# Kernel tuning notes

Hardware: AMD Instinct MI355X
Metric: run time of the kernel (lower is better)

The kernel has to match this reference:

```python
import jax, jax.numpy as jnp
import numpy as np
from jax import lax

B, S, H = 2, 2048, 768
FF = 1536
E = 8
TOP_K = 2


def setup_inputs() -> dict:
    key = jax.random.key(0)
    k1, k2, k3, k4 = jax.random.split(key, 4)
    hidden_states = jax.random.normal(k1, (B, S, H), dtype=jnp.float32)
    # torch init: weight.normal_() for experts; nn.Linear default init for gate (approx normal here is fine for a numerics baseline)
    gate_w = jax.random.normal(k2, (E, H), dtype=jnp.float32) * 0.02
    w_fc = jax.random.normal(k3, (E, FF, H), dtype=jnp.float32) * 0.02
    w_proj = jax.random.normal(k4, (E, H, FF), dtype=jnp.float32) * 0.02
    return {"hidden_states": hidden_states, "gate_w": gate_w, "w_fc": w_fc, "w_proj": w_proj}


def reference(hidden_states, gate_w, w_fc, w_proj):
    b, s, h = hidden_states.shape
    x = hidden_states.reshape(-1, h)                      # [T, H]
    # --- top-k gating (logits in float32, as in the torch code) ---
    logits = (x @ gate_w.T).astype(jnp.float32)           # [T, E]
    top_logits, top_idx = lax.top_k(logits, TOP_K)        # [T, K]
    gates = jax.nn.softmax(top_logits, axis=1).astype(x.dtype)  # [T, K]
    # combined per-token/per-expert gate: g[t,e] = sum_k gates[t,k]*[idx[t,k]==e]
    onehot = jax.nn.one_hot(top_idx, E, dtype=x.dtype)    # [T, K, E]
    g = jnp.einsum('tk,tke->te', gates, onehot)           # [T, E]
    # --- experts: gather + per-expert GEMM + gated scatter-add combine ---
    # Equivalent math: tokens with zero gate for expert e contribute nothing,
    # so compute each expert on all tokens and weight by g[:, e].
    out = jnp.zeros_like(x)
    for e in range(E):  # fixed small loop over experts (structurally distinct weights)
        hmid = jax.nn.gelu(x @ w_fc[e].T, approximate=False)   # [T, FF] (torch gelu = erf form)
        out = out + g[:, e:e + 1] * (hmid @ w_proj[e].T)       # [T, H]
    out = out.reshape(b, s, h)
    return out, logits
```

## Files before the change

kernel.cpp:

```cpp
#include <hip/hip_runtime.h>
#include <hip/hip_bf16.h>
#include <math.h>
#include <stdint.h>

#define TOKENS 4096
#define HDIM   768
#define FFDIM  1536
#define NEXP   8
#define MAXRT  72

typedef __attribute__((ext_vector_type(8))) short bf16x8;
typedef __attribute__((ext_vector_type(4))) float f32x4;

__device__ __forceinline__ unsigned short f2bf(float f) {
    union { float f; uint32_t u; } c; c.f = f;
    uint32_t u = c.u;
    uint32_t r = (u + 0x7FFFu + ((u >> 16) & 1u)) >> 16;
    return (unsigned short)r;
}

__device__ __forceinline__ void gload_lds16(const void* g, void* l) {
    __builtin_amdgcn_global_load_lds(
        (const __attribute__((address_space(1))) void*)g,
        (__attribute__((address_space(3))) void*)l, 16, 0, 0);
}

__global__ void cast_bf16_2(const float* __restrict__ s1, unsigned short* __restrict__ d1,
                            const float* __restrict__ s2, unsigned short* __restrict__ d2,
                            int n4) {
    int stride = gridDim.x * blockDim.x;
    for (int i = blockIdx.x * blockDim.x + threadIdx.x; i < 2 * n4; i += stride) {
        const float4* s = (i < n4) ? (const float4*)s1 : (const float4*)s2;
        ushort4* d = (i < n4) ? (ushort4*)d1 : (ushort4*)d2;
        int j = (i < n4) ? i : i - n4;
        float4 v = s[j];
        ushort4 o;
        o.x = f2bf(v.x); o.y = f2bf(v.y); o.z = f2bf(v.z); o.w = f2bf(v.w);
        d[j] = o;
    }
}

__global__ __launch_bounds__(256) void gating(
    const float* __restrict__ x, const float* __restrict__ gw,
    float* __restrict__ logits,
    int* __restrict__ tok_e, float* __restrict__ tok_g,
    unsigned short* __restrict__ x_bf, float* __restrict__ outp)
{
    float4 zz = make_float4(0.f, 0.f, 0.f, 0.f);
#pragma unroll
    for (int j = 0; j < 3; j++)
        ((float4*)outp)[blockIdx.x * 768 + j * 256 + threadIdx.x] = zz;

    int t = blockIdx.x * 4 + (threadIdx.x >> 6);
    int lane = threadIdx.x & 63;
    const float4* xt = (const float4*)(x + (size_t)t * HDIM);
    const float4* gw4 = (const float4*)gw;
    ushort4* xbt = (ushort4*)(x_bf + (size_t)t * HDIM);
    float acc[NEXP];
#pragma unroll
    for (int e = 0; e < NEXP; e++) acc[e] = 0.f;
#pragma unroll
    for (int it = 0; it < 3; it++) {
        int i = lane + it * 64;
        float4 xv = xt[i];
        ushort4 o;
        o.x = f2bf(xv.x); o.y = f2bf(xv.y); o.z = f2bf(xv.z); o.w = f2bf(xv.w);
        xbt[i] = o;
#pragma unroll
        for (int e = 0; e < NEXP; e++) {
            float4 wv = gw4[e * 192 + i];
            acc[e] += xv.x * wv.x + xv.y * wv.y + xv.z * wv.z + xv.w * wv.w;
        }
    }
#pragma unroll
    for (int e = 0; e < NEXP; e++) {
#pragma unroll
        for (int off = 32; off > 0; off >>= 1)
            acc[e] += __shfl_xor(acc[e], off);
    }
    if (lane == 0) {
        float4 l0 = make_float4(acc[0], acc[1], acc[2], acc[3]);
        float4 l1 = make_float4(acc[4], acc[5], acc[6], acc[7]);
        float4* lp = (float4*)(logits + (size_t)t * NEXP);
        lp[0] = l0; lp[1] = l1;
        int i0 = 0; float v0 = acc[0];
#pragma unroll
        for (int e = 1; e < NEXP; e++) if (acc[e] > v0) { v0 = acc[e]; i0 = e; }
        int i1 = -1; float v1 = -3.4e38f;
#pragma unroll
        for (int e = 0; e < NEXP; e++) if (e != i0 && acc[e] > v1) { v1 = acc[e]; i1 = e; }
        float g0 = 1.f / (1.f + expf(v1 - v0));
        tok_e[t * 2] = i0; tok_e[t * 2 + 1] = i1;
        tok_g[t * 2] = g0; tok_g[t * 2 + 1] = 1.f - g0;
    }
}

__global__ __launch_bounds__(1024) void build_lists(
    const int* __restrict__ tok_e, const float* __restrict__ tok_g,
    int* __restrict__ counts, int* __restrict__ bases,
    int* __restrict__ rtiles, int* __restrict__ nrt,
    int* __restrict__ entries, float* __restrict__ gates)
{
    __shared__ unsigned long long wlo[16], whi[16];
    int tid = threadIdx.x;
    int lane = tid & 63, wid = tid >> 6;
    int eL[8]; float gL[8];
    int4 ea = ((const int4*)tok_e)[tid * 2];
    int4 eb = ((const int4*)tok_e)[tid * 2 + 1];
    float4 ga = ((const float4*)tok_g)[tid * 2];
    float4 gb = ((const float4*)tok_g)[tid * 2 + 1];
    eL[0] = ea.x; eL[1] = ea.y; eL[2] = ea.z; eL[3] = ea.w;
    eL[4] = eb.x; eL[5] = eb.y; eL[6] = eb.z; eL[7] = eb.w;
    gL[0] = ga.x; gL[1] = ga.y; gL[2] = ga.z; gL[3] = ga.w;
    gL[4] = gb.x; gL[5] = gb.y; gL[6] = gb.z; gL[7] = gb.w;

    unsigned long long clo = 0, chi = 0;
#pragma unroll
    for (int j = 0; j < 8; j++) {
        int e = eL[j];
        unsigned long long one = 1ull << ((e & 3) * 16);
        if (e < 4) clo += one; else chi += one;
    }
    unsigned long long ilo = clo, ihi = chi;
#pragma unroll
    for (int s = 1; s < 64; s <<= 1) {
        unsigned long long t1 = __shfl_up(ilo, s);
        unsigned long long t2 = __shfl_up(ihi, s);
        if (lane >= s) { ilo += t1; ihi += t2; }
    }
    if (lane == 63) { wlo[wid] = ilo; whi[wid] = ihi; }
    __syncthreads();
    if (tid == 0) {
        unsigned long long rl = 0, rh = 0;
#pragma unroll
        for (int i = 0; i < 16; i++) {
            unsigned long long a = wlo[i], b = whi[i];
            wlo[i] = rl; whi[i] = rh;
            rl += a; rh += b;
        }
        int c[8];
#pragma unroll
        for (int e = 0; e < 4; e++) {
            c[e]     = (int)((rl >> (e * 16)) & 0xFFFF);
            c[e + 4] = (int)((rh >> (e * 16)) & 0xFFFF);
        }
        int b = 0, nt = 0;
#pragma unroll
        for (int e = 0; e < NEXP; e++) {
            counts[e] = c[e]; bases[e] = b; b += c[e];
            for (int r = 0; r < c[e]; r += 128) rtiles[nt++] = (e << 16) | r;
        }
        nrt[0] = nt;
    }
    __syncthreads();
    unsigned long long rlo = wlo[wid] + (ilo - clo);
    unsigned long long rhi = whi[wid] + (ihi - chi);
#pragma unroll
    for (int j = 0; j < 8; j++) {
        int e = eL[j];
        int sh = (e & 3) * 16;
        unsigned long long one = 1ull << sh;
        int slot;
        if (e < 4) { slot = (int)((rlo >> sh) & 0xFFFF); rlo += one; }
        else       { slot = (int)((rhi >> sh) & 0xFFFF); rhi += one; }
        entries[e * TOKENS + slot] = tid * 8 + j;
        gates[e * TOKENS + slot]   = gL[j];
    }
}

template<int KD, int ND, int TN, bool IS_FC>
__global__ __launch_bounds__(256) void moe_gemm(
    const unsigned short* __restrict__ Asrc,
    const unsigned short* __restrict__ Bsrc,
    const int* __restrict__ counts,
    const int* __restrict__ bases,
    const int* __restrict__ rtiles,
    const int* __restrict__ nrt,
    const int* __restrict__ entries,
    const float* __restrict__ gates,
    unsigned short* __restrict__ hmid,
    float* __restrict__ outp)
{
    constexpr int AJ = TN / 32;
    constexpr int CB = TN / 32;
    int ti = blockIdx.y;
    if (ti >= nrt[0]) return;
    int pk   = rtiles[ti];
    int e    = pk >> 16;
    int row0 = pk & 0xFFFF;
    int n_e  = counts[e];
    int ebase = bases[e];
    int n0 = blockIdx.x * TN;

    __shared__ __align__(16) unsigned short sA[128 * 64];
    __shared__ __align__(16) unsigned short sB[TN * 64];

    int tid = threadIdx.x;
    int w = tid >> 6;
    int l = tid & 63;
    const int* lst = entries + e * TOKENS;

    int sg = l & 7;
    int lr8 = l >> 3;
    const unsigned short* Ag[4];
    int aLds[4];
#pragma unroll
    for (int c = 0; c < 4; c++) {
        int rr = w * 32 + c * 8 + lr8;
        int gr = row0 + rr;
        int id = gr < n_e ? gr : n_e - 1;
        size_t arow = IS_FC ? (size_t)(lst[id] >> 1) : (size_t)(ebase + id);
        Ag[c] = Asrc + arow * KD + (size_t)((sg ^ (rr & 7)) * 8);
        aLds[c] = (w * 32 + c * 8) * 64;
    }
    const unsigned short* Bg[CB];
    int bLds[CB];
#pragma unroll
    for (int c = 0; c < CB; c++) {
        int rr = w * (TN / 4) + c * 8 + lr8;
        Bg[c] = Bsrc + ((size_t)e * ND + n0 + rr) * KD + (size_t)((sg ^ (rr & 7)) * 8);
        bLds[c] = (w * (TN / 4) + c * 8) * 64;
    }

    int lo = l & 15;
    int q  = l >> 4;
    int wr = w >> 1, wc = w & 1;
    int aOff[4][2], bOff[AJ][2];
#pragma unroll
    for (int i = 0; i < 4; i++) {
        int m = wr * 64 + i * 16 + lo;
#pragma unroll
        for (int s = 0; s < 2; s++)
            aOff[i][s] = m * 64 + ((s * 4 + q) ^ (m & 7)) * 8;
    }
#pragma unroll
    for (int j = 0; j < AJ; j++) {
        int n = wc * (TN / 2) + j * 16 + lo;
#pragma unroll
        for (int s = 0; s < 2; s++)
            bOff[j][s] = n * 64 + ((s * 4 + q) ^ (n & 7)) * 8;
    }

    f32x4 acc[4][AJ];
#pragma unroll
    for (int i = 0; i < 4; i++)
#pragma unroll
        for (int j = 0; j < AJ; j++) acc[i][j] = (f32x4){0.f, 0.f, 0.f, 0.f};

    for (int k0 = 0; k0 < KD; k0 += 64) {
#pragma unroll
        for (int c = 0; c < 4; c++) gload_lds16(Ag[c] + k0, sA + aLds[c]);
#pragma unroll
        for (int c = 0; c < CB; c++) gload_lds16(Bg[c] + k0, sB + bLds[c]);
        __syncthreads();
#pragma unroll
        for (int s = 0; s < 2; s++) {
            bf16x8 a[4], b[AJ];
#pragma unroll
            for (int i = 0; i < 4; i++) a[i] = *(const bf16x8*)(sA + aOff[i][s]);
#pragma unroll
            for (int j = 0; j < AJ; j++) b[j] = *(const bf16x8*)(sB + bOff[j][s]);
#pragma unroll
            for (int i = 0; i < 4; i++)
#pragma unroll
                for (int j = 0; j < AJ; j++)
                    acc[i][j] = __builtin_amdgcn_mfma_f32_16x16x32_bf16(a[i], b[j], acc[i][j], 0, 0, 0);
        }
        __syncthreads();
    }

#pragma unroll
    for (int i = 0; i < 4; i++) {
        int rowB = row0 + wr * 64 + i * 16 + q * 4;
#pragma unroll
        for (int rr = 0; rr < 4; rr++) {
            int orow = rowB + rr;
            if (orow < n_e) {
                if (IS_FC) {
                    size_t hrow = (size_t)(ebase + orow);
#pragma unroll
                    for (int j = 0; j < AJ; j++) {
                        float v = acc[i][j][rr];
                        v = 0.5f * v * (1.f + erff(v * 0.70710678118654752f));
                        hmid[hrow * ND + n0 + wc * (TN / 2) + j * 16 + lo] = f2bf(v);
                    }
                } else {
                    int token = lst[orow] >> 1;
                    float g = gates[e * TOKENS + orow];
#pragma unroll
                    for (int j = 0; j < AJ; j++) {
                        atomicAdd(&outp[(size_t)token * ND + n0 + wc * (TN / 2) + j * 16 + lo],
                                  acc[i][j][rr] * g);
                    }
                }
            }
        }
    }
}

extern "C" void kernel_launch(void* const* d_in, const int* in_sizes, int n_in,
                              void* d_out, int out_size, void* d_ws, size_t ws_size,
                              hipStream_t stream) {
    const float* x     = (const float*)d_in[0];
    const float* gw    = (const float*)d_in[1];
    const float* wfc   = (const float*)d_in[2];
    const float* wproj = (const float*)d_in[3];
    float* outp   = (float*)d_out;
    float* logits = outp + (size_t)TOKENS * HDIM;

    char* ws = (char*)d_ws;
    int*   counts  = (int*)ws;
    int*   bases   = (int*)(ws + 64);
    int*   nrt     = (int*)(ws + 128);
    int*   rtiles  = (int*)(ws + 160);
    int*   entries = (int*)(ws + 512);
    float* gates   = (float*)(ws + 512 + NEXP * TOKENS * 4);
    size_t off = 512 + 2ull * NEXP * TOKENS * 4;
    int*   tok_e   = (int*)(ws + off);   off += (size_t)TOKENS * 2 * 4;
    float* tok_g   = (float*)(ws + off); off += (size_t)TOKENS * 2 * 4;
    unsigned short* x_bf   = (unsigned short*)(ws + off); off += (size_t)TOKENS * HDIM * 2;
    unsigned short* wfc_bf = (unsigned short*)(ws + off); off += (size_t)NEXP * FFDIM * HDIM * 2;
    unsigned short* wpj_bf = (unsigned short*)(ws + off); off += (size_t)NEXP * HDIM * FFDIM * 2;
    unsigned short* hmid   = (unsigned short*)(ws + off);

    cast_bf16_2<<<2048, 256, 0, stream>>>(wfc, wfc_bf, wproj, wpj_bf,
                                          NEXP * FFDIM * HDIM / 4);
    gating<<<TOKENS / 4, 256, 0, stream>>>(x, gw, logits, tok_e, tok_g, x_bf, outp);
    build_lists<<<1, 1024, 0, stream>>>(tok_e, tok_g, counts, bases, rtiles, nrt,
                                        entries, gates);
    moe_gemm<HDIM, FFDIM, 128, true ><<<dim3(FFDIM / 128, MAXRT), 256, 0, stream>>>(
        x_bf, wfc_bf, counts, bases, rtiles, nrt, entries, gates, hmid, outp);
    moe_gemm<FFDIM, HDIM, 64, false><<<dim3(HDIM / 64, MAXRT), 256, 0, stream>>>(
        hmid, wpj_bf, counts, bases, rtiles, nrt, entries, gates, hmid, outp);
}
```

Measured before the change: 241.0 us.

## Schedule GEMM tiles via XCD-aware work list to group expert weights per XCD

Replaces the 2D (column-tile, row-tile) grid with a flat 1D grid indexed into a precomputed work list. Work items are interleaved with stride 8, so workgroups dispatched round-robin to the same XCD get tiles from the same expert. The aim is better L2 reuse of each expert's weights and fewer wasted blocks. This adds serial scheduling work in the single-thread build_lists section and launches a fixed 2048 blocks, most of which exit early.

```diff
diff --git a/kernel.cpp b/kernel.cpp
--- a/kernel.cpp
+++ b/kernel.cpp
@@ -7,7 +7,8 @@
 #define HDIM   768
 #define FFDIM  1536
 #define NEXP   8
-#define MAXRT  72
+#define NCT    12
+#define WMAX   256
 
 typedef __attribute__((ext_vector_type(8))) short bf16x8;
 typedef __attribute__((ext_vector_type(4))) float f32x4;
@@ -98,12 +99,15 @@
 __global__ __launch_bounds__(1024) void build_lists(
     const int* __restrict__ tok_e, const float* __restrict__ tok_g,
     int* __restrict__ counts, int* __restrict__ bases,
-    int* __restrict__ rtiles, int* __restrict__ nrt,
+    int* __restrict__ work,
     int* __restrict__ entries, float* __restrict__ gates)
 {
     __shared__ unsigned long long wlo[16], whi[16];
     int tid = threadIdx.x;
     int lane = tid & 63, wid = tid >> 6;
+#pragma unroll
+    for (int j = 0; j < (8 * WMAX) / 1024; j++) work[j * 1024 + tid] = -1;
+
     int eL[8]; float gL[8];
     int4 ea = ((const int4*)tok_e)[tid * 2];
     int4 eb = ((const int4*)tok_e)[tid * 2 + 1];
@@ -144,13 +148,24 @@
             c[e]     = (int)((rl >> (e * 16)) & 0xFFFF);
             c[e + 4] = (int)((rh >> (e * 16)) & 0xFFFF);
         }
-        int b = 0, nt = 0;
-#pragma unroll
+        int b = 0;
+        int blen[8];
+#pragma unroll
+        for (int e = 0; e < NEXP; e++) { counts[e] = c[e]; bases[e] = b; b += c[e]; blen[e] = 0; }
         for (int e = 0; e < NEXP; e++) {
-            counts[e] = c[e]; bases[e] = b; b += c[e];
-            for (int r = 0; r < c[e]; r += 128) rtiles[nt++] = (e << 16) | r;
-        }
-        nrt[0] = nt;
+            int rts = (c[e] + 127) >> 7;
+            for (int ct = 0; ct < NCT; ct++) {
+                for (int r = 0; r < rts; r++) {
+                    int bk = e;
+                    if (blen[bk] >= WMAX) {
+                        int mn = 0x7FFFFFFF;
+                        for (int k = 0; k < 8; k++) if (blen[k] < mn) { mn = blen[k]; bk = k; }
+                    }
+                    work[blen[bk] * 8 + bk] = (ct << 20) | (e << 16) | (r << 7);
+                    blen[bk]++;
+                }
+            }
+        }
     }
     __syncthreads();
     unsigned long long rlo = wlo[wid] + (ilo - clo);
@@ -174,8 +189,7 @@
     const unsigned short* __restrict__ Bsrc,
     const int* __restrict__ counts,
     const int* __restrict__ bases,
-    const int* __restrict__ rtiles,
-    const int* __restrict__ nrt,
+    const int* __restrict__ work,
     const int* __restrict__ entries,
     const float* __restrict__ gates,
     unsigned short* __restrict__ hmid,
@@ -183,14 +197,14 @@
 {
     constexpr int AJ = TN / 32;
     constexpr int CB = TN / 32;
-    int ti = blockIdx.y;
-    if (ti >= nrt[0]) return;
-    int pk   = rtiles[ti];
-    int e    = pk >> 16;
+    int pk = work[blockIdx.x];
+    if (pk < 0) return;
+    int ct   = pk >> 20;
+    int e    = (pk >> 16) & 0xF;
     int row0 = pk & 0xFFFF;
     int n_e  = counts[e];
     int ebase = bases[e];
-    int n0 = blockIdx.x * TN;
+    int n0 = ct * TN;
 
     __shared__ __align__(16) unsigned short sA[128 * 64];
     __shared__ __align__(16) unsigned short sB[TN * 64];
@@ -311,11 +325,10 @@
     char* ws = (char*)d_ws;
     int*   counts  = (int*)ws;
     int*   bases   = (int*)(ws + 64);
-    int*   nrt     = (int*)(ws + 128);
-    int*   rtiles  = (int*)(ws + 160);
-    int*   entries = (int*)(ws + 512);
-    float* gates   = (float*)(ws + 512 + NEXP * TOKENS * 4);
-    size_t off = 512 + 2ull * NEXP * TOKENS * 4;
+    int*   work    = (int*)(ws + 128);
+    int*   entries = (int*)(ws + 128 + 8 * WMAX * 4);
+    float* gates   = (float*)(ws + 128 + 8 * WMAX * 4 + NEXP * TOKENS * 4);
+    size_t off = 128 + 8 * WMAX * 4 + 2ull * NEXP * TOKENS * 4;
     int*   tok_e   = (int*)(ws + off);   off += (size_t)TOKENS * 2 * 4;
     float* tok_g   = (float*)(ws + off); off += (size_t)TOKENS * 2 * 4;
     unsigned short* x_bf   = (unsigned short*)(ws + off); off += (size_t)TOKENS * HDIM * 2;
@@ -326,10 +339,10 @@
     cast_bf16_2<<<2048, 256, 0, stream>>>(wfc, wfc_bf, wproj, wpj_bf,
                                           NEXP * FFDIM * HDIM / 4);
     gating<<<TOKENS / 4, 256, 0, stream>>>(x, gw, logits, tok_e, tok_g, x_bf, outp);
-    build_lists<<<1, 1024, 0, stream>>>(tok_e, tok_g, counts, bases, rtiles, nrt,
+    build_lists<<<1, 1024, 0, stream>>>(tok_e, tok_g, counts, bases, work,
                                         entries, gates);
-    moe_gemm<HDIM, FFDIM, 128, true ><<<dim3(FFDIM / 128, MAXRT), 256, 0, stream>>>(
-        x_bf, wfc_bf, counts, bases, rtiles, nrt, entries, gates, hmid, outp);
-    moe_gemm<FFDIM, HDIM, 64, false><<<dim3(HDIM / 64, MAXRT), 256, 0, stream>>>(
-        hmid, wpj_bf, counts, bases, rtiles, nrt, entries, gates, hmid, outp);
-}
+    moe_gemm<HDIM, FFDIM, 128, true ><<<8 * WMAX, 256, 0, stream>>>(
+        x_bf, wfc_bf, counts, bases, work, entries, gates, hmid, outp);
+    moe_gemm<FFDIM, HDIM, 64, false><<<8 * WMAX, 256, 0, stream>>>(
+        hmid, wpj_bf, counts, bases, work, entries, gates, hmid, outp);
+}
```

Result: slower. 324.9 us (+34.8%).
